# Performance work log

Measured on AMD Instinct MI355X. Metric: run time of the kernel, lower is better.

## Reference

```python
import jax, jax.numpy as jnp
import numpy as np

N, E = 100000, 1600000
IN_C, HID, NUM_CLASSES = 128, 256, 15
EPS = 1e-5


def setup_inputs() -> dict:
    key = jax.random.key(0)
    ks = jax.random.split(key, 20)

    def lin(k, out_c, in_c):
        # torch Linear default init: U(-1/sqrt(in), 1/sqrt(in))
        bound = 1.0 / np.sqrt(in_c)
        return jax.random.uniform(k, (out_c, in_c), jnp.float32, -bound, bound)

    inp = {
        'x': jax.random.normal(ks[0], (N, IN_C), jnp.float32),
        'edge_index': jax.random.randint(ks[1], (2, E), 0, N, jnp.int64),
        # conv1: SAGEConv(IN_C -> HID): lin_l (with bias) on aggregated msgs, lin_r (no bias) on root
        'w1_l': lin(ks[2], HID, IN_C), 'b1_l': jnp.zeros((HID,), jnp.float32), 'w1_r': lin(ks[3], HID, IN_C),
        'g1': jnp.ones((HID,), jnp.float32), 'be1': jnp.zeros((HID,), jnp.float32),
        # conv2: HID -> HID
        'w2_l': lin(ks[4], HID, HID), 'b2_l': jnp.zeros((HID,), jnp.float32), 'w2_r': lin(ks[5], HID, HID),
        'g2': jnp.ones((HID,), jnp.float32), 'be2': jnp.zeros((HID,), jnp.float32),
        # conv3: HID -> HID//2
        'w3_l': lin(ks[6], HID // 2, HID), 'b3_l': jnp.zeros((HID // 2,), jnp.float32), 'w3_r': lin(ks[7], HID // 2, HID),
        'g3': jnp.ones((HID // 2,), jnp.float32), 'be3': jnp.zeros((HID // 2,), jnp.float32),
        # classifier
        'wc': lin(ks[8], NUM_CLASSES, HID // 2), 'bc': jnp.zeros((NUM_CLASSES,), jnp.float32),
    }
    return inp


def _sage(x, src, dst, w_l, b_l, w_r):
    # PyG SAGEConv (aggr='mean'): lin_l(mean_{j in N(i)} x_j) + lin_r(x_i)
    n = x.shape[0]
    agg = jax.ops.segment_sum(x[src], dst, num_segments=n)            # [N, d]
    deg = jax.ops.segment_sum(jnp.ones_like(dst, dtype=x.dtype), dst, num_segments=n)
    mean = agg / jnp.maximum(deg, 1.0)[:, None]
    return mean @ w_l.T + b_l + x @ w_r.T


def _bn_relu(x, g, b):
    # BatchNorm1d in training mode: biased batch stats over node dim, then ReLU
    mu = jnp.mean(x, axis=0)
    var = jnp.mean((x - mu) ** 2, axis=0)
    return jax.nn.relu((x - mu) * jax.lax.rsqrt(var + EPS) * g + b)


def reference(x, edge_index, w1_l, b1_l, w1_r, g1, be1, w2_l, b2_l, w2_r, g2, be2,
              w3_l, b3_l, w3_r, g3, be3, wc, bc):
    src, dst = edge_index[0], edge_index[1]
    h = _bn_relu(_sage(x, src, dst, w1_l, b1_l, w1_r), g1, be1)   # dropout = identity (eval)
    h = _bn_relu(_sage(h, src, dst, w2_l, b2_l, w2_r), g2, be2)
    h = _bn_relu(_sage(h, src, dst, w3_l, b3_l, w3_r), g3, be3)
    return h @ wc.T + bc
```

## Files before the change

kernel.cpp:

```cpp
#include <hip/hip_runtime.h>


#define DEV static __device__ __forceinline__

typedef unsigned short us;
typedef __attribute__((ext_vector_type(8))) __bf16 bf16x8;
typedef __attribute__((ext_vector_type(4))) float f32x4;

DEV float bf2f(us u) { return __uint_as_float(((unsigned)u) << 16); }
DEV us f2bf(float f) {
    unsigned u = __float_as_uint(f);
    unsigned r = u + 0x7fffu + ((u >> 16) & 1u);
    return (us)(r >> 16);
}

typedef __attribute__((address_space(3))) void lds_void;
typedef const __attribute__((address_space(1))) void gbl_void;
DEV void gll16(const void* g, void* l) {
    __builtin_amdgcn_global_load_lds((gbl_void*)g, (lds_void*)l, 16, 0, 0);
}

DEV bool is_i64(const int* ei) {
    return (ei[1] == 0) & (ei[3] == 0) & (ei[5] == 0) & (ei[7] == 0);
}


__global__ void bucket_hist(const int* __restrict__ ei, int E, int* __restrict__ hist2,
                            int NB, int chunk) {
    __shared__ int h[256];
    const int g = blockIdx.x, t = threadIdx.x;
    const bool i64 = is_i64(ei);
    h[t] = 0;
    __syncthreads();
    int beg = g * chunk, end = min(beg + chunk, E);
    for (int e = beg + t; e < end; e += 256) {
        int d = i64 ? ei[2 * (E + e)] : ei[E + e];
        atomicAdd(&h[d >> 9], 1);
    }
    __syncthreads();
    if (t < NB) hist2[g * NB + t] = h[t];
}

__global__ void bucket_offsets(int* __restrict__ hist2, int* __restrict__ bucketBase,
                               int* __restrict__ rp, int N, int G, int NB) {
    __shared__ int tot[256];
    const int t = threadIdx.x;
    int sum = 0;
    if (t < NB)
        for (int g = 0; g < G; ++g) sum += hist2[g * NB + t];
    tot[t] = sum;
    __syncthreads();
    for (int off = 1; off < 256; off <<= 1) {
        int v = (t >= off) ? tot[t - off] : 0;
        __syncthreads();
        tot[t] += v;
        __syncthreads();
    }
    int base = tot[t] - sum;
    if (t < NB) {
        bucketBase[t] = base;
        int run = base;
        for (int g = 0; g < G; ++g) {
            int v = hist2[g * NB + t];
            hist2[g * NB + t] = run;
            run += v;
        }
        if (t == NB - 1) {
            bucketBase[NB] = tot[t];
            rp[N] = tot[t];
        }
    }
}

__global__ void scatter8(const int* __restrict__ ei, int E, const int* __restrict__ hist2,
                         uint2* __restrict__ ebuf, int NB, int chunk) {
    __shared__ int off[256];
    const int g = blockIdx.x, t = threadIdx.x;
    const bool i64 = is_i64(ei);
    if (t < NB) off[t] = hist2[g * NB + t];
    __syncthreads();
    int beg = g * chunk, end = min(beg + chunk, E);
    for (int e = beg + t; e < end; e += 256) {
        int s = i64 ? ei[2 * e] : ei[e];
        int d = i64 ? ei[2 * (E + e)] : ei[E + e];
        int p = atomicAdd(&off[d >> 9], 1);
        ebuf[p] = make_uint2((unsigned)s, (unsigned)d);
    }
}

__global__ void fine_csr(const uint2* __restrict__ ebuf, const int* __restrict__ bucketBase,
                         int N, int* __restrict__ rp, int* __restrict__ csr) {
    __shared__ int cnt[512];
    __shared__ int red[256];
    const int b = blockIdx.x, t = threadIdx.x;
    const int node0 = b << 9;
    cnt[t] = 0;
    cnt[t + 256] = 0;
    __syncthreads();
    const int ebeg = bucketBase[b], eend = bucketBase[b + 1];
    for (int e = ebeg + t; e < eend; e += 256) {
        uint2 r = ebuf[e];
        atomicAdd(&cnt[r.y & 511], 1);
    }
    __syncthreads();
    int c0 = cnt[2 * t], c1 = cnt[2 * t + 1];
    int s = c0 + c1;
    red[t] = s;
    __syncthreads();
    for (int off = 1; off < 256; off <<= 1) {
        int v = (t >= off) ? red[t - off] : 0;
        __syncthreads();
        red[t] += v;
        __syncthreads();
    }
    int pre = red[t] - s;
    int n0 = node0 + 2 * t;
    if (n0 < N) rp[n0] = ebeg + pre;
    if (n0 + 1 < N) rp[n0 + 1] = ebeg + pre + c0;
    __syncthreads();
    cnt[2 * t] = ebeg + pre;
    cnt[2 * t + 1] = ebeg + pre + c0;
    __syncthreads();
    for (int e = ebeg + t; e < eend; e += 256) {
        uint2 r = ebuf[e];
        int p = atomicAdd(&cnt[r.y & 511], 1);
        csr[p] = (int)r.x;
    }
}


struct WSeg { const float* s; us* d; int n4; int l2w4; int stride; };
struct WConvAll { WSeg seg[8]; };

__global__ void conv_all(WConvAll wc) {
    for (int sg = 0; sg < 8; ++sg) {
        WSeg w = wc.seg[sg];
        for (int i = blockIdx.x * blockDim.x + threadIdx.x; i < w.n4; i += gridDim.x * blockDim.x) {
            float4 v = ((const float4*)w.s)[i];
            ushort4 r;
            r.x = f2bf(v.x); r.y = f2bf(v.y); r.z = f2bf(v.z); r.w = f2bf(v.w);
            int row = i >> w.l2w4;
            int col = (i - (row << w.l2w4)) * 4;
            *(ushort4*)(w.d + (size_t)row * w.stride + col) = r;
        }
    }
}


template <int VEC>
__global__ void agg_mean(const us* __restrict__ X, const int* __restrict__ rp,
                         const int* __restrict__ csr, us* __restrict__ M, int n) {
    const int cols = VEC * 64;
    int w = blockIdx.x * (blockDim.x >> 6) + (threadIdx.x >> 6);
    int lane = threadIdx.x & 63;
    if (w >= n) return;
    int beg = rp[w], end = rp[w + 1];
    const us* Xb = X + lane * VEC;
    float acc[VEC];
#pragma unroll
    for (int i = 0; i < VEC; ++i) acc[i] = 0.f;
    int e = beg;
    for (; e + 4 <= end; e += 4) {
        int j0 = csr[e], j1 = csr[e + 1], j2 = csr[e + 2], j3 = csr[e + 3];
        if (VEC == 2) {
            unsigned u0 = *(const unsigned*)(Xb + (size_t)j0 * cols);
            unsigned u1 = *(const unsigned*)(Xb + (size_t)j1 * cols);
            unsigned u2 = *(const unsigned*)(Xb + (size_t)j2 * cols);
            unsigned u3 = *(const unsigned*)(Xb + (size_t)j3 * cols);
            acc[0] += __uint_as_float(u0 << 16) + __uint_as_float(u1 << 16)
                    + __uint_as_float(u2 << 16) + __uint_as_float(u3 << 16);
            acc[1] += __uint_as_float(u0 & 0xffff0000u) + __uint_as_float(u1 & 0xffff0000u)
                    + __uint_as_float(u2 & 0xffff0000u) + __uint_as_float(u3 & 0xffff0000u);
        } else {
            uint2 u0 = *(const uint2*)(Xb + (size_t)j0 * cols);
            uint2 u1 = *(const uint2*)(Xb + (size_t)j1 * cols);
            uint2 u2 = *(const uint2*)(Xb + (size_t)j2 * cols);
            uint2 u3 = *(const uint2*)(Xb + (size_t)j3 * cols);
            acc[0] += __uint_as_float(u0.x << 16) + __uint_as_float(u1.x << 16)
                    + __uint_as_float(u2.x << 16) + __uint_as_float(u3.x << 16);
            acc[1] += __uint_as_float(u0.x & 0xffff0000u) + __uint_as_float(u1.x & 0xffff0000u)
                    + __uint_as_float(u2.x & 0xffff0000u) + __uint_as_float(u3.x & 0xffff0000u);
            acc[2] += __uint_as_float(u0.y << 16) + __uint_as_float(u1.y << 16)
                    + __uint_as_float(u2.y << 16) + __uint_as_float(u3.y << 16);
            acc[3] += __uint_as_float(u0.y & 0xffff0000u) + __uint_as_float(u1.y & 0xffff0000u)
                    + __uint_as_float(u2.y & 0xffff0000u) + __uint_as_float(u3.y & 0xffff0000u);
        }
    }
    for (; e < end; ++e) {
        int j0 = csr[e];
        if (VEC == 2) {
            unsigned u0 = *(const unsigned*)(Xb + (size_t)j0 * cols);
            acc[0] += __uint_as_float(u0 << 16);
            acc[1] += __uint_as_float(u0 & 0xffff0000u);
        } else {
            uint2 u0 = *(const uint2*)(Xb + (size_t)j0 * cols);
            acc[0] += __uint_as_float(u0.x << 16);
            acc[1] += __uint_as_float(u0.x & 0xffff0000u);
            acc[2] += __uint_as_float(u0.y << 16);
            acc[3] += __uint_as_float(u0.y & 0xffff0000u);
        }
    }
    float inv = 1.0f / (float)max(end - beg, 1);
    us* q = M + (size_t)w * cols + lane * VEC;
    if (VEC == 2) {
        *(ushort2*)q = make_ushort2(f2bf(acc[0] * inv), f2bf(acc[1] * inv));
    } else {
        *(ushort4*)q = make_ushort4(f2bf(acc[0] * inv), f2bf(acc[1] * inv),
                                    f2bf(acc[2] * inv), f2bf(acc[3] * inv));
    }
}

__global__ void agg_post(const us* __restrict__ Yc, const int* __restrict__ rp,
                         const int* __restrict__ csr, const float* __restrict__ bias,
                         us* __restrict__ H, int n) {
    int w = blockIdx.x * (blockDim.x >> 6) + (threadIdx.x >> 6);
    int lane = threadIdx.x & 63;
    if (w >= n) return;
    int beg = rp[w], end = rp[w + 1];
    const us* Yb = Yc + lane * 2;
    float a0 = 0.f, a1 = 0.f;
    int e = beg;
    for (; e + 4 <= end; e += 4) {
        int j0 = csr[e], j1 = csr[e + 1], j2 = csr[e + 2], j3 = csr[e + 3];
        unsigned u0 = *(const unsigned*)(Yb + (size_t)j0 * 256);
        unsigned u1 = *(const unsigned*)(Yb + (size_t)j1 * 256);
        unsigned u2 = *(const unsigned*)(Yb + (size_t)j2 * 256);
        unsigned u3 = *(const unsigned*)(Yb + (size_t)j3 * 256);
        a0 += __uint_as_float(u0 << 16) + __uint_as_float(u1 << 16)
            + __uint_as_float(u2 << 16) + __uint_as_float(u3 << 16);
        a1 += __uint_as_float(u0 & 0xffff0000u) + __uint_as_float(u1 & 0xffff0000u)
            + __uint_as_float(u2 & 0xffff0000u) + __uint_as_float(u3 & 0xffff0000u);
    }
    for (; e < end; ++e) {
        unsigned u0 = *(const unsigned*)(Yb + (size_t)csr[e] * 256);
        a0 += __uint_as_float(u0 << 16);
        a1 += __uint_as_float(u0 & 0xffff0000u);
    }
    float inv = 1.0f / (float)max(end - beg, 1);
    unsigned uz = *(const unsigned*)(Yc + (size_t)w * 256 + 128 + lane * 2);
    float2 bv = *(const float2*)(bias + lane * 2);
    float r0 = a0 * inv + __uint_as_float(uz << 16) + bv.x;
    float r1 = a1 * inv + __uint_as_float(uz & 0xffff0000u) + bv.y;
    *(ushort2*)(H + (size_t)w * 128 + lane * 2) = make_ushort2(f2bf(r0), f2bf(r1));
}


template <int THREADS, int BM, int BN, int WM, int WN>
__launch_bounds__(THREADS)
__global__ void gemm_mfma(const us* __restrict__ A0, int K0,
                          const us* __restrict__ A1, int K1,
                          const us* __restrict__ W, const float* __restrict__ bias,
                          int n, int outc, us* __restrict__ Cbf, float* __restrict__ Cf,
                          float* __restrict__ st0, float* __restrict__ st1) {
    constexpr int MT = WM / 16;
    constexpr int NT = WN / 16;
    constexpr int WCols = BN / WN;
    constexpr int NDMA = (BM * 4 + BN * 4) / THREADS;
    static_assert((BM * 4) % THREADS == 0 && (BN * 4) % THREADS == 0, "uniform DMA");
    static_assert((BM / WM) * (BN / WN) == THREADS / 64, "wave tiling");
    __shared__ __align__(16) us As[2][BM * 32];
    __shared__ __align__(16) us Bs[2][BN * 32];
    __shared__ float colred[2][BN];

    const int t = threadIdx.x;
    const int wid = t >> 6, lane = t & 63;
    const int wr = wid / WCols, wcc = wid % WCols;
    const int row0 = blockIdx.x * BM;
    const int col0 = blockIdx.y * BN;
    const int Kp = K0 + K1;
    const int nk = Kp >> 5;
    const int l15 = lane & 15, l4 = lane >> 4;

    auto issue = [&](int kidx, int p) {
        int kc = kidx << 5;
        const us* A = (kc < K0) ? A0 : A1;
        int rs = (kc < K0) ? K0 : K1;
        int ko = (kc < K0) ? kc : kc - K0;
#pragma unroll
        for (int c = t; c < BM * 4; c += THREADS) {
            int blk = c >> 6;
            int row = row0 + (blk << 4) + l15;
            gll16(A + (size_t)row * rs + ko + (l4 << 3), (char*)As[p] + blk * 1024 + lane * 16);
        }
#pragma unroll
        for (int c = t; c < BN * 4; c += THREADS) {
            int blk = c >> 6;
            int col = col0 + (blk << 4) + l15;
            gll16(W + (size_t)col * Kp + kc + (l4 << 3), (char*)Bs[p] + blk * 1024 + lane * 16);
        }
    };

    f32x4 acc[MT][NT];
#pragma unroll
    for (int i = 0; i < MT; ++i)
#pragma unroll
        for (int j = 0; j < NT; ++j) acc[i][j] = (f32x4){0.f, 0.f, 0.f, 0.f};

    issue(0, 0);
    if (nk > 1) issue(1, 1);
    for (int k = 0; k < nk; ++k) {
        if (k + 1 < nk) asm volatile("s_waitcnt vmcnt(%0)" :: "i"(NDMA) : "memory");
        else            asm volatile("s_waitcnt vmcnt(0)" ::: "memory");
        asm volatile("s_barrier" ::: "memory");
        const int p = k & 1;
        bf16x8 af[MT], bfr[NT];
#pragma unroll
        for (int mt = 0; mt < MT; ++mt)
            af[mt] = *(const bf16x8*)((char*)As[p] + (wr * MT + mt) * 1024 + lane * 16);
#pragma unroll
        for (int nt = 0; nt < NT; ++nt)
            bfr[nt] = *(const bf16x8*)((char*)Bs[p] + (wcc * NT + nt) * 1024 + lane * 16);
#pragma unroll
        for (int mt = 0; mt < MT; ++mt)
#pragma unroll
            for (int nt = 0; nt < NT; ++nt)
                acc[mt][nt] = __builtin_amdgcn_mfma_f32_16x16x32_bf16(af[mt], bfr[nt], acc[mt][nt], 0, 0, 0);
        if (k + 2 < nk) {
            asm volatile("s_barrier" ::: "memory");
            issue(k + 2, p);
        }
    }

    if (st0) {
#pragma unroll
        for (int c = t; c < 2 * BN; c += THREADS) (&colred[0][0])[c] = 0.f;
        __syncthreads();
    }

#pragma unroll
    for (int nt = 0; nt < NT; ++nt) {
        int col = col0 + wcc * WN + nt * 16 + l15;
        bool cok = col < outc;
        float bv = (bias != nullptr && cok) ? bias[col] : 0.f;
        float ls = 0.f, lq = 0.f;
#pragma unroll
        for (int mt = 0; mt < MT; ++mt) {
            int rbase = row0 + wr * WM + mt * 16 + (l4 << 2);
#pragma unroll
            for (int i = 0; i < 4; ++i) {
                int r = rbase + i;
                if (r < n && cok) {
                    float v = acc[mt][nt][i] + bv;
                    if (Cf) Cf[(size_t)r * outc + col] = v;
                    else Cbf[(size_t)r * outc + col] = f2bf(v);
                    ls += v;
                    lq += v * v;
                }
            }
        }
        if (st0 && cok) {
            int lc = wcc * WN + nt * 16 + l15;
            atomicAdd(&colred[0][lc], ls);
            atomicAdd(&colred[1][lc], lq);
        }
    }
    if (st0) {
        __syncthreads();
        int rep = (blockIdx.x & 7) << 8;
        for (int c = t; c < BN; c += THREADS) {
            if (col0 + c < outc) {
                atomicAdd(&st0[rep + col0 + c], colred[0][c]);
                atomicAdd(&st1[rep + col0 + c], colred[1][c]);
            }
        }
    }
}


__global__ void bn_stats(const us* __restrict__ H, int n, int c,
                         float* __restrict__ s0, float* __restrict__ s1) {
    int col = threadIdx.x;
    if (col >= c) return;
    float s = 0.f, q = 0.f;
    for (int r = blockIdx.x; r < n; r += gridDim.x) {
        float v = bf2f(H[(size_t)r * c + col]);
        s += v;
        q += v * v;
    }
    int rep = (blockIdx.x & 7) << 8;
    atomicAdd(&s0[rep + col], s);
    atomicAdd(&s1[rep + col], q);
}

__global__ void bn_apply(us* __restrict__ H, int n8, int c,
                         const float* __restrict__ s0, const float* __restrict__ s1,
                         const float* __restrict__ g, const float* __restrict__ be, float fn) {
    __shared__ float sc[256], sh[256];
    int t = threadIdx.x;
    if (t < c) {
        float s = 0.f, q = 0.f;
#pragma unroll
        for (int r = 0; r < 8; ++r) {
            s += s0[(r << 8) + t];
            q += s1[(r << 8) + t];
        }
        float mean = s / fn;
        float var = q / fn - mean * mean;
        float scale = g[t] * rsqrtf(var + 1e-5f);
        sc[t] = scale;
        sh[t] = be[t] - mean * scale;
    }
    __syncthreads();
    int cdiv8 = c >> 3;
    for (int i = blockIdx.x * blockDim.x + t; i < n8; i += gridDim.x * blockDim.x) {
        int col = (i % cdiv8) << 3;
        uint4 v = ((const uint4*)H)[i];
        float f[8];
        f[0] = __uint_as_float(v.x << 16); f[1] = __uint_as_float(v.x & 0xffff0000u);
        f[2] = __uint_as_float(v.y << 16); f[3] = __uint_as_float(v.y & 0xffff0000u);
        f[4] = __uint_as_float(v.z << 16); f[5] = __uint_as_float(v.z & 0xffff0000u);
        f[6] = __uint_as_float(v.w << 16); f[7] = __uint_as_float(v.w & 0xffff0000u);
        float4 sc0 = *(const float4*)&sc[col];
        float4 sc1 = *(const float4*)&sc[col + 4];
        float4 sh0 = *(const float4*)&sh[col];
        float4 sh1 = *(const float4*)&sh[col + 4];
        f[0] = fmaxf(f[0] * sc0.x + sh0.x, 0.f);
        f[1] = fmaxf(f[1] * sc0.y + sh0.y, 0.f);
        f[2] = fmaxf(f[2] * sc0.z + sh0.z, 0.f);
        f[3] = fmaxf(f[3] * sc0.w + sh0.w, 0.f);
        f[4] = fmaxf(f[4] * sc1.x + sh1.x, 0.f);
        f[5] = fmaxf(f[5] * sc1.y + sh1.y, 0.f);
        f[6] = fmaxf(f[6] * sc1.z + sh1.z, 0.f);
        f[7] = fmaxf(f[7] * sc1.w + sh1.w, 0.f);
        uint4 o;
        o.x = (unsigned)f2bf(f[0]) | ((unsigned)f2bf(f[1]) << 16);
        o.y = (unsigned)f2bf(f[2]) | ((unsigned)f2bf(f[3]) << 16);
        o.z = (unsigned)f2bf(f[4]) | ((unsigned)f2bf(f[5]) << 16);
        o.w = (unsigned)f2bf(f[6]) | ((unsigned)f2bf(f[7]) << 16);
        ((uint4*)H)[i] = o;
    }
}


extern "C" void kernel_launch(void* const* d_in, const int* in_sizes, int n_in,
                              void* d_out, int out_size, void* d_ws, size_t ws_size,
                              hipStream_t stream) {
    const float* x = (const float*)d_in[0];
    const int* ei = (const int*)d_in[1];
    const float* w1_l = (const float*)d_in[2];
    const float* b1_l = (const float*)d_in[3];
    const float* w1_r = (const float*)d_in[4];
    const float* g1 = (const float*)d_in[5];
    const float* be1 = (const float*)d_in[6];
    const float* w2_l = (const float*)d_in[7];
    const float* b2_l = (const float*)d_in[8];
    const float* w2_r = (const float*)d_in[9];
    const float* g2 = (const float*)d_in[10];
    const float* be2 = (const float*)d_in[11];
    const float* w3_l = (const float*)d_in[12];
    const float* b3_l = (const float*)d_in[13];
    const float* w3_r = (const float*)d_in[14];
    const float* g3 = (const float*)d_in[15];
    const float* be3 = (const float*)d_in[16];
    const float* wcf = (const float*)d_in[17];
    const float* bc = (const float*)d_in[18];

    const int N = in_sizes[0] / 128;
    const int E = in_sizes[1] / 2;
    const int NB = (N + 511) >> 9;
    const int G = 256;
    const int chunk = (E + G - 1) / G;

    char* ws = (char*)d_ws;
    size_t off = 0;
    auto alloc = [&](size_t bytes) -> char* {
        char* p = ws + off;
        off += (bytes + 255) & ~(size_t)255;
        return p;
    };
    int* rp = (int*)alloc((size_t)(N + 1) * 4);
    int* csr = (int*)alloc((size_t)E * 4);
    int* hist2 = (int*)alloc((size_t)G * NB * 4);
    int* bucketBase = (int*)alloc((size_t)(NB + 1) * 4);
    uint2* ebuf = (uint2*)alloc((size_t)E * 8);
    us* xbf = (us*)alloc((size_t)N * 128 * 2);
    us* M = (us*)alloc((size_t)N * 256 * 2);
    us* Ha = (us*)alloc((size_t)N * 256 * 2);
    us* Hb = (us*)alloc((size_t)N * 256 * 2);
    float* stats = (float*)alloc(6 * 8 * 256 * 4);
    float* s01 = stats,          *s11 = stats + 2048;
    float* s02 = stats + 4096,   *s12 = stats + 6144;
    float* s03 = stats + 8192,   *s13 = stats + 10240;
    us* wcat1 = (us*)alloc(256 * 256 * 2);
    us* wcat2 = (us*)alloc(256 * 512 * 2);
    us* w3cat = (us*)alloc(256 * 256 * 2);
    us* wc_b = (us*)alloc(64 * 128 * 2);
    alloc(1 << 20);
    (void)ws_size; (void)n_in; (void)out_size;

    hipMemsetAsync(stats, 0, 6 * 8 * 256 * 4, stream);
    WConvAll wc;
    wc.seg[0] = {x,    xbf,         N * 128 / 4,  5, 128};
    wc.seg[1] = {w1_l, wcat1,       256 * 128 / 4, 5, 256};
    wc.seg[2] = {w1_r, wcat1 + 128, 256 * 128 / 4, 5, 256};
    wc.seg[3] = {w2_l, wcat2,       256 * 256 / 4, 6, 512};
    wc.seg[4] = {w2_r, wcat2 + 256, 256 * 256 / 4, 6, 512};
    wc.seg[5] = {w3_l, w3cat,             128 * 256 / 4, 6, 256};
    wc.seg[6] = {w3_r, w3cat + 128 * 256, 128 * 256 / 4, 6, 256};
    wc.seg[7] = {wcf,  wc_b,        15 * 128 / 4,  5, 128};
    conv_all<<<1024, 256, 0, stream>>>(wc);
    bucket_hist<<<G, 256, 0, stream>>>(ei, E, hist2, NB, chunk);
    bucket_offsets<<<1, 256, 0, stream>>>(hist2, bucketBase, rp, N, G, NB);
    scatter8<<<G, 256, 0, stream>>>(ei, E, hist2, ebuf, NB, chunk);
    fine_csr<<<NB, 256, 0, stream>>>(ebuf, bucketBase, N, rp, csr);

    const int aggGrid = (N + 3) / 4;
    const int rowTiles = (N + 127) / 128;

    agg_mean<2><<<aggGrid, 256, 0, stream>>>(xbf, rp, csr, M, N);
    gemm_mfma<512, 128, 256, 64, 64><<<rowTiles, 512, 0, stream>>>(
        M, 128, xbf, 128, wcat1, b1_l, N, 256, Ha, nullptr, s01, s11);
    bn_apply<<<2048, 256, 0, stream>>>(Ha, N * 256 / 8, 256, s01, s11, g1, be1, (float)N);

    agg_mean<4><<<aggGrid, 256, 0, stream>>>(Ha, rp, csr, M, N);
    gemm_mfma<512, 128, 256, 64, 64><<<rowTiles, 512, 0, stream>>>(
        M, 256, Ha, 256, wcat2, b2_l, N, 256, Hb, nullptr, s02, s12);
    bn_apply<<<2048, 256, 0, stream>>>(Hb, N * 256 / 8, 256, s02, s12, g2, be2, (float)N);

    gemm_mfma<512, 128, 256, 64, 64><<<rowTiles, 512, 0, stream>>>(
        Hb, 256, nullptr, 0, w3cat, nullptr, N, 256, M, nullptr, nullptr, nullptr);
    agg_post<<<aggGrid, 256, 0, stream>>>(M, rp, csr, b3_l, Ha, N);
    bn_stats<<<1024, 256, 0, stream>>>(Ha, N, 128, s03, s13);
    bn_apply<<<2048, 256, 0, stream>>>(Ha, N * 128 / 8, 128, s03, s13, g3, be3, (float)N);

    gemm_mfma<256, 128, 64, 128, 16><<<rowTiles, 256, 0, stream>>>(
        Ha, 128, nullptr, 0, wc_b, bc, N, 15, nullptr, (float*)d_out, nullptr, nullptr);
}
```

Measured before the change: 797.9 us.

## Fuse BN stats into agg_post, merge prep kernels, software-pipeline gathers

```diff
diff --git a/kernel.cpp b/kernel.cpp
--- a/kernel.cpp
+++ b/kernel.cpp
@@ -24,22 +24,54 @@
     return (ei[1] == 0) & (ei[3] == 0) & (ei[5] == 0) & (ei[7] == 0);
 }
 
-
-__global__ void bucket_hist(const int* __restrict__ ei, int E, int* __restrict__ hist2,
-                            int NB, int chunk) {
+DEV void rowacc2(float* acc, unsigned u) {
+    acc[0] += __uint_as_float(u << 16);
+    acc[1] += __uint_as_float(u & 0xffff0000u);
+}
+DEV void rowacc4(float* acc, uint2 u) {
+    acc[0] += __uint_as_float(u.x << 16);
+    acc[1] += __uint_as_float(u.x & 0xffff0000u);
+    acc[2] += __uint_as_float(u.y << 16);
+    acc[3] += __uint_as_float(u.y & 0xffff0000u);
+}
+
+
+struct WSeg { const float* s; us* d; int n4; int l2w4; int stride; };
+struct WConvAll { WSeg seg[8]; };
+
+
+__global__ void prep0(WConvAll wc, const int* __restrict__ ei, int E,
+                      int* __restrict__ hist2, int NB, int chunk) {
     __shared__ int h[256];
-    const int g = blockIdx.x, t = threadIdx.x;
-    const bool i64 = is_i64(ei);
-    h[t] = 0;
-    __syncthreads();
-    int beg = g * chunk, end = min(beg + chunk, E);
-    for (int e = beg + t; e < end; e += 256) {
-        int d = i64 ? ei[2 * (E + e)] : ei[E + e];
-        atomicAdd(&h[d >> 9], 1);
-    }
-    __syncthreads();
-    if (t < NB) hist2[g * NB + t] = h[t];
-}
+    const int t = threadIdx.x;
+    if (blockIdx.x < 256) {
+        const int g = blockIdx.x;
+        const bool i64 = is_i64(ei);
+        h[t] = 0;
+        __syncthreads();
+        int beg = g * chunk, end = min(beg + chunk, E);
+        for (int e = beg + t; e < end; e += 256) {
+            int d = i64 ? ei[2 * (E + e)] : ei[E + e];
+            atomicAdd(&h[d >> 9], 1);
+        }
+        __syncthreads();
+        if (t < NB) hist2[g * NB + t] = h[t];
+    } else {
+        const int bid = blockIdx.x - 256;
+        for (int sg = 0; sg < 8; ++sg) {
+            WSeg w = wc.seg[sg];
+            for (int i = bid * 256 + t; i < w.n4; i += 1024 * 256) {
+                float4 v = ((const float4*)w.s)[i];
+                ushort4 r;
+                r.x = f2bf(v.x); r.y = f2bf(v.y); r.z = f2bf(v.z); r.w = f2bf(v.w);
+                int row = i >> w.l2w4;
+                int col = (i - (row << w.l2w4)) * 4;
+                *(ushort4*)(w.d + (size_t)row * w.stride + col) = r;
+            }
+        }
+    }
+}
+
 
 __global__ void bucket_offsets(int* __restrict__ hist2, int* __restrict__ bucketBase,
                                int* __restrict__ rp, int N, int G, int NB) {
@@ -125,24 +157,6 @@
         uint2 r = ebuf[e];
         int p = atomicAdd(&cnt[r.y & 511], 1);
         csr[p] = (int)r.x;
-    }
-}
-
-
-struct WSeg { const float* s; us* d; int n4; int l2w4; int stride; };
-struct WConvAll { WSeg seg[8]; };
-
-__global__ void conv_all(WConvAll wc) {
-    for (int sg = 0; sg < 8; ++sg) {
-        WSeg w = wc.seg[sg];
-        for (int i = blockIdx.x * blockDim.x + threadIdx.x; i < w.n4; i += gridDim.x * blockDim.x) {
-            float4 v = ((const float4*)w.s)[i];
-            ushort4 r;
-            r.x = f2bf(v.x); r.y = f2bf(v.y); r.z = f2bf(v.z); r.w = f2bf(v.w);
-            int row = i >> w.l2w4;
-            int col = (i - (row << w.l2w4)) * 4;
-            *(ushort4*)(w.d + (size_t)row * w.stride + col) = r;
-        }
     }
 }
 
@@ -160,47 +174,53 @@
 #pragma unroll
     for (int i = 0; i < VEC; ++i) acc[i] = 0.f;
     int e = beg;
-    for (; e + 4 <= end; e += 4) {
-        int j0 = csr[e], j1 = csr[e + 1], j2 = csr[e + 2], j3 = csr[e + 3];
-        if (VEC == 2) {
-            unsigned u0 = *(const unsigned*)(Xb + (size_t)j0 * cols);
-            unsigned u1 = *(const unsigned*)(Xb + (size_t)j1 * cols);
-            unsigned u2 = *(const unsigned*)(Xb + (size_t)j2 * cols);
-            unsigned u3 = *(const unsigned*)(Xb + (size_t)j3 * cols);
-            acc[0] += __uint_as_float(u0 << 16) + __uint_as_float(u1 << 16)
-                    + __uint_as_float(u2 << 16) + __uint_as_float(u3 << 16);
-            acc[1] += __uint_as_float(u0 & 0xffff0000u) + __uint_as_float(u1 & 0xffff0000u)
-                    + __uint_as_float(u2 & 0xffff0000u) + __uint_as_float(u3 & 0xffff0000u);
-        } else {
-            uint2 u0 = *(const uint2*)(Xb + (size_t)j0 * cols);
-            uint2 u1 = *(const uint2*)(Xb + (size_t)j1 * cols);
-            uint2 u2 = *(const uint2*)(Xb + (size_t)j2 * cols);
-            uint2 u3 = *(const uint2*)(Xb + (size_t)j3 * cols);
-            acc[0] += __uint_as_float(u0.x << 16) + __uint_as_float(u1.x << 16)
-                    + __uint_as_float(u2.x << 16) + __uint_as_float(u3.x << 16);
-            acc[1] += __uint_as_float(u0.x & 0xffff0000u) + __uint_as_float(u1.x & 0xffff0000u)
-                    + __uint_as_float(u2.x & 0xffff0000u) + __uint_as_float(u3.x & 0xffff0000u);
-            acc[2] += __uint_as_float(u0.y << 16) + __uint_as_float(u1.y << 16)
-                    + __uint_as_float(u2.y << 16) + __uint_as_float(u3.y << 16);
-            acc[3] += __uint_as_float(u0.y & 0xffff0000u) + __uint_as_float(u1.y & 0xffff0000u)
-                    + __uint_as_float(u2.y & 0xffff0000u) + __uint_as_float(u3.y & 0xffff0000u);
-        }
-    }
-    for (; e < end; ++e) {
-        int j0 = csr[e];
-        if (VEC == 2) {
-            unsigned u0 = *(const unsigned*)(Xb + (size_t)j0 * cols);
-            acc[0] += __uint_as_float(u0 << 16);
-            acc[1] += __uint_as_float(u0 & 0xffff0000u);
-        } else {
-            uint2 u0 = *(const uint2*)(Xb + (size_t)j0 * cols);
-            acc[0] += __uint_as_float(u0.x << 16);
-            acc[1] += __uint_as_float(u0.x & 0xffff0000u);
-            acc[2] += __uint_as_float(u0.y << 16);
-            acc[3] += __uint_as_float(u0.y & 0xffff0000u);
-        }
-    }
-    float inv = 1.0f / (float)max(end - beg, 1);
+    int cnt = end - beg;
+    if (VEC == 2) {
+        if (cnt >= 8) {
+            int j[4];
+            unsigned u[4], un[4];
+#pragma unroll
+            for (int q = 0; q < 4; ++q) j[q] = csr[e + q];
+#pragma unroll
+            for (int q = 0; q < 4; ++q) u[q] = *(const unsigned*)(Xb + (size_t)j[q] * cols);
+            for (e = beg + 4; e + 4 <= end; e += 4) {
+#pragma unroll
+                for (int q = 0; q < 4; ++q) j[q] = csr[e + q];
+#pragma unroll
+                for (int q = 0; q < 4; ++q) un[q] = *(const unsigned*)(Xb + (size_t)j[q] * cols);
+#pragma unroll
+                for (int q = 0; q < 4; ++q) rowacc2(acc, u[q]);
+#pragma unroll
+                for (int q = 0; q < 4; ++q) u[q] = un[q];
+            }
+#pragma unroll
+            for (int q = 0; q < 4; ++q) rowacc2(acc, u[q]);
+        }
+        for (; e < end; ++e) rowacc2(acc, *(const unsigned*)(Xb + (size_t)csr[e] * cols));
+    } else {
+        if (cnt >= 8) {
+            int j[4];
+            uint2 u[4], un[4];
+#pragma unroll
+            for (int q = 0; q < 4; ++q) j[q] = csr[e + q];
+#pragma unroll
+            for (int q = 0; q < 4; ++q) u[q] = *(const uint2*)(Xb + (size_t)j[q] * cols);
+            for (e = beg + 4; e + 4 <= end; e += 4) {
+#pragma unroll
+                for (int q = 0; q < 4; ++q) j[q] = csr[e + q];
+#pragma unroll
+                for (int q = 0; q < 4; ++q) un[q] = *(const uint2*)(Xb + (size_t)j[q] * cols);
+#pragma unroll
+                for (int q = 0; q < 4; ++q) rowacc4(acc, u[q]);
+#pragma unroll
+                for (int q = 0; q < 4; ++q) u[q] = un[q];
+            }
+#pragma unroll
+            for (int q = 0; q < 4; ++q) rowacc4(acc, u[q]);
+        }
+        for (; e < end; ++e) rowacc4(acc, *(const uint2*)(Xb + (size_t)csr[e] * cols));
+    }
+    float inv = 1.0f / (float)max(cnt, 1);
     us* q = M + (size_t)w * cols + lane * VEC;
     if (VEC == 2) {
         *(ushort2*)q = make_ushort2(f2bf(acc[0] * inv), f2bf(acc[1] * inv));
@@ -212,36 +232,58 @@
 
 __global__ void agg_post(const us* __restrict__ Yc, const int* __restrict__ rp,
                          const int* __restrict__ csr, const float* __restrict__ bias,
-                         us* __restrict__ H, int n) {
-    int w = blockIdx.x * (blockDim.x >> 6) + (threadIdx.x >> 6);
-    int lane = threadIdx.x & 63;
-    if (w >= n) return;
-    int beg = rp[w], end = rp[w + 1];
-    const us* Yb = Yc + lane * 2;
-    float a0 = 0.f, a1 = 0.f;
-    int e = beg;
-    for (; e + 4 <= end; e += 4) {
-        int j0 = csr[e], j1 = csr[e + 1], j2 = csr[e + 2], j3 = csr[e + 3];
-        unsigned u0 = *(const unsigned*)(Yb + (size_t)j0 * 256);
-        unsigned u1 = *(const unsigned*)(Yb + (size_t)j1 * 256);
-        unsigned u2 = *(const unsigned*)(Yb + (size_t)j2 * 256);
-        unsigned u3 = *(const unsigned*)(Yb + (size_t)j3 * 256);
-        a0 += __uint_as_float(u0 << 16) + __uint_as_float(u1 << 16)
-            + __uint_as_float(u2 << 16) + __uint_as_float(u3 << 16);
-        a1 += __uint_as_float(u0 & 0xffff0000u) + __uint_as_float(u1 & 0xffff0000u)
-            + __uint_as_float(u2 & 0xffff0000u) + __uint_as_float(u3 & 0xffff0000u);
-    }
-    for (; e < end; ++e) {
-        unsigned u0 = *(const unsigned*)(Yb + (size_t)csr[e] * 256);
-        a0 += __uint_as_float(u0 << 16);
-        a1 += __uint_as_float(u0 & 0xffff0000u);
-    }
-    float inv = 1.0f / (float)max(end - beg, 1);
-    unsigned uz = *(const unsigned*)(Yc + (size_t)w * 256 + 128 + lane * 2);
-    float2 bv = *(const float2*)(bias + lane * 2);
-    float r0 = a0 * inv + __uint_as_float(uz << 16) + bv.x;
-    float r1 = a1 * inv + __uint_as_float(uz & 0xffff0000u) + bv.y;
-    *(ushort2*)(H + (size_t)w * 128 + lane * 2) = make_ushort2(f2bf(r0), f2bf(r1));
+                         us* __restrict__ H, int n,
+                         float* __restrict__ s0, float* __restrict__ s1) {
+    __shared__ float cr[2][128];
+    const int t = threadIdx.x;
+    ((float*)cr)[t] = 0.f;
+    __syncthreads();
+    int w = blockIdx.x * (blockDim.x >> 6) + (t >> 6);
+    int lane = t & 63;
+    if (w < n) {
+        int beg = rp[w], end = rp[w + 1];
+        const us* Yb = Yc + lane * 2;
+        float acc[2] = {0.f, 0.f};
+        int e = beg;
+        int cnt = end - beg;
+        if (cnt >= 8) {
+            int j[4];
+            unsigned u[4], un[4];
+#pragma unroll
+            for (int q = 0; q < 4; ++q) j[q] = csr[e + q];
+#pragma unroll
+            for (int q = 0; q < 4; ++q) u[q] = *(const unsigned*)(Yb + (size_t)j[q] * 256);
+            for (e = beg + 4; e + 4 <= end; e += 4) {
+#pragma unroll
+                for (int q = 0; q < 4; ++q) j[q] = csr[e + q];
+#pragma unroll
+                for (int q = 0; q < 4; ++q) un[q] = *(const unsigned*)(Yb + (size_t)j[q] * 256);
+#pragma unroll
+                for (int q = 0; q < 4; ++q) rowacc2(acc, u[q]);
+#pragma unroll
+                for (int q = 0; q < 4; ++q) u[q] = un[q];
+            }
+#pragma unroll
+            for (int q = 0; q < 4; ++q) rowacc2(acc, u[q]);
+        }
+        for (; e < end; ++e) rowacc2(acc, *(const unsigned*)(Yb + (size_t)csr[e] * 256));
+        float inv = 1.0f / (float)max(cnt, 1);
+        unsigned uz = *(const unsigned*)(Yc + (size_t)w * 256 + 128 + lane * 2);
+        float2 bv = *(const float2*)(bias + lane * 2);
+        float r0 = acc[0] * inv + __uint_as_float(uz << 16) + bv.x;
+        float r1 = acc[1] * inv + __uint_as_float(uz & 0xffff0000u) + bv.y;
+        us b0 = f2bf(r0), b1 = f2bf(r1);
+        *(ushort2*)(H + (size_t)w * 128 + lane * 2) = make_ushort2(b0, b1);
+        float v0 = bf2f(b0), v1 = bf2f(b1);
+        atomicAdd(&cr[0][2 * lane], v0);
+        atomicAdd(&cr[1][2 * lane], v0 * v0);
+        atomicAdd(&cr[0][2 * lane + 1], v1);
+        atomicAdd(&cr[1][2 * lane + 1], v1 * v1);
+    }
+    __syncthreads();
+    int rep = (blockIdx.x & 15) << 7;
+    if (t < 128) atomicAdd(&s0[rep + t], cr[0][t]);
+    else atomicAdd(&s1[rep + (t - 128)], cr[1][t - 128]);
 }
 
 
@@ -367,32 +409,17 @@
 }
 
 
-__global__ void bn_stats(const us* __restrict__ H, int n, int c,
-                         float* __restrict__ s0, float* __restrict__ s1) {
-    int col = threadIdx.x;
-    if (col >= c) return;
-    float s = 0.f, q = 0.f;
-    for (int r = blockIdx.x; r < n; r += gridDim.x) {
-        float v = bf2f(H[(size_t)r * c + col]);
-        s += v;
-        q += v * v;
-    }
-    int rep = (blockIdx.x & 7) << 8;
-    atomicAdd(&s0[rep + col], s);
-    atomicAdd(&s1[rep + col], q);
-}
-
 __global__ void bn_apply(us* __restrict__ H, int n8, int c,
                          const float* __restrict__ s0, const float* __restrict__ s1,
-                         const float* __restrict__ g, const float* __restrict__ be, float fn) {
+                         const float* __restrict__ g, const float* __restrict__ be, float fn,
+                         int reps, int rstride) {
     __shared__ float sc[256], sh[256];
     int t = threadIdx.x;
     if (t < c) {
         float s = 0.f, q = 0.f;
-#pragma unroll
-        for (int r = 0; r < 8; ++r) {
-            s += s0[(r << 8) + t];
-            q += s1[(r << 8) + t];
+        for (int r = 0; r < reps; ++r) {
+            s += s0[r * rstride + t];
+            q += s1[r * rstride + t];
         }
         float mean = s / fn;
         float var = q / fn - mean * mean;
@@ -498,8 +525,7 @@
     wc.seg[5] = {w3_l, w3cat,             128 * 256 / 4, 6, 256};
     wc.seg[6] = {w3_r, w3cat + 128 * 256, 128 * 256 / 4, 6, 256};
     wc.seg[7] = {wcf,  wc_b,        15 * 128 / 4,  5, 128};
-    conv_all<<<1024, 256, 0, stream>>>(wc);
-    bucket_hist<<<G, 256, 0, stream>>>(ei, E, hist2, NB, chunk);
+    prep0<<<1280, 256, 0, stream>>>(wc, ei, E, hist2, NB, chunk);
     bucket_offsets<<<1, 256, 0, stream>>>(hist2, bucketBase, rp, N, G, NB);
     scatter8<<<G, 256, 0, stream>>>(ei, E, hist2, ebuf, NB, chunk);
     fine_csr<<<NB, 256, 0, stream>>>(ebuf, bucketBase, N, rp, csr);
@@ -510,18 +536,17 @@
     agg_mean<2><<<aggGrid, 256, 0, stream>>>(xbf, rp, csr, M, N);
     gemm_mfma<512, 128, 256, 64, 64><<<rowTiles, 512, 0, stream>>>(
         M, 128, xbf, 128, wcat1, b1_l, N, 256, Ha, nullptr, s01, s11);
-    bn_apply<<<2048, 256, 0, stream>>>(Ha, N * 256 / 8, 256, s01, s11, g1, be1, (float)N);
+    bn_apply<<<2048, 256, 0, stream>>>(Ha, N * 256 / 8, 256, s01, s11, g1, be1, (float)N, 8, 256);
 
     agg_mean<4><<<aggGrid, 256, 0, stream>>>(Ha, rp, csr, M, N);
     gemm_mfma<512, 128, 256, 64, 64><<<rowTiles, 512, 0, stream>>>(
         M, 256, Ha, 256, wcat2, b2_l, N, 256, Hb, nullptr, s02, s12);
-    bn_apply<<<2048, 256, 0, stream>>>(Hb, N * 256 / 8, 256, s02, s12, g2, be2, (float)N);
+    bn_apply<<<2048, 256, 0, stream>>>(Hb, N * 256 / 8, 256, s02, s12, g2, be2, (float)N, 8, 256);
 
     gemm_mfma<512, 128, 256, 64, 64><<<rowTiles, 512, 0, stream>>>(
         Hb, 256, nullptr, 0, w3cat, nullptr, N, 256, M, nullptr, nullptr, nullptr);
-    agg_post<<<aggGrid, 256, 0, stream>>>(M, rp, csr, b3_l, Ha, N);
-    bn_stats<<<1024, 256, 0, stream>>>(Ha, N, 128, s03, s13);
-    bn_apply<<<2048, 256, 0, stream>>>(Ha, N * 128 / 8, 128, s03, s13, g3, be3, (float)N);
+    agg_post<<<aggGrid, 256, 0, stream>>>(M, rp, csr, b3_l, Ha, N, s03, s13);
+    bn_apply<<<2048, 256, 0, stream>>>(Ha, N * 128 / 8, 128, s03, s13, g3, be3, (float)N, 16, 128);
 
     gemm_mfma<256, 128, 64, 128, 16><<<rowTiles, 256, 0, stream>>>(
         Ha, 128, nullptr, 0, wc_b, bc, N, 15, nullptr, (float*)d_out, nullptr, nullptr);
```

Result: slower. 857.1 us (+7.4%).
